# Kernel tuning notes

Hardware: AMD Instinct MI355X
Metric: run time of the kernel (lower is better)

The kernel has to match this reference:

```python
import jax, jax.numpy as jnp
import numpy as np

EMBED = 1024
HEADS = 16
HEAD_DIM = EMBED // HEADS
B, T = 2, 2048


def setup_inputs() -> dict:
    key = jax.random.key(0)
    k1, k2, k3, k4, k5 = jax.random.split(key, 5)
    x = jax.random.normal(k1, (B, T, EMBED), dtype=jnp.float32)
    Wq = jax.random.normal(k2, (HEADS, EMBED, HEAD_DIM), dtype=jnp.float32)
    Wk = jax.random.normal(k3, (HEADS, EMBED, HEAD_DIM), dtype=jnp.float32)
    Wv = jax.random.normal(k4, (HEADS, EMBED, HEAD_DIM), dtype=jnp.float32)
    # nn.Linear weight is [out_features, in_features]
    Wo = jax.random.normal(k5, (EMBED, EMBED), dtype=jnp.float32) * (1.0 / np.sqrt(EMBED))
    return {"x": x, "Wq": Wq, "Wk": Wk, "Wv": Wv, "Wo": Wo}


def reference(x, Wq, Wk, Wv, Wo):
    b, t, e = x.shape
    h, _, i = Wq.shape
    q = jnp.einsum('hei,bte->hbti', Wq, x)
    k = jnp.einsum('hei,bte->hbti', Wk, x)
    v = jnp.einsum('hei,bte->hbti', Wv, x)
    # NOTE: original module scales by sqrt(seq_len), not sqrt(head_dim)
    fit = jnp.einsum('hbti,hbsi->hbts', q, k) / jnp.sqrt(jnp.float32(t))
    fit = jax.nn.softmax(fit, axis=-1)
    attended = jnp.einsum('hbts,hbsi->hbti', fit, v)
    # rearrange 'h b t i -> b t (h i)'
    attended = attended.transpose(1, 2, 0, 3).reshape(b, t, h * i)
    return attended @ Wo.T
```

## Files before the change

### kernel.cpp

```cpp
#include <hip/hip_runtime.h>
#include <math.h>

#define E_DIM 1024
#define H_NUM 16
#define HD 64
#define B_NUM 2
#define T_LEN 2048

typedef unsigned short u16;
typedef short bf16x8 __attribute__((ext_vector_type(8)));
typedef float f32x4 __attribute__((ext_vector_type(4)));
typedef unsigned short u16x4 __attribute__((ext_vector_type(4)));
typedef unsigned short u16x8 __attribute__((ext_vector_type(8)));
typedef unsigned int u32x2 __attribute__((ext_vector_type(2)));

#define MFMA16(a, b, c) __builtin_amdgcn_mfma_f32_16x16x32_bf16(a, b, c, 0, 0, 0)

__device__ __forceinline__ u16 f2bf(float f) {
    unsigned u = __float_as_uint(f);
    u += 0x7FFFu + ((u >> 16) & 1u);
    return (u16)(u >> 16);
}
__device__ __forceinline__ float bf2f(u16 b) {
    return __uint_as_float(((unsigned)b) << 16);
}
__device__ __forceinline__ void gl_lds16(const void* g, void* l) {
    __builtin_amdgcn_global_load_lds(
        (const __attribute__((address_space(1))) unsigned int*)g,
        (__attribute__((address_space(3))) unsigned int*)l, 16, 0, 0);
}


__global__ __launch_bounds__(256) void convert_x_kernel(
    const float* __restrict__ x, u16* __restrict__ xh, u16* __restrict__ xl)
{
    int i = (blockIdx.x * 256 + threadIdx.x) * 4;
    float4 f = *(const float4*)&x[i];
    float fv[4] = {f.x, f.y, f.z, f.w};
    u16x4 h, l;
    #pragma unroll
    for (int j = 0; j < 4; j++) {
        u16 hi = f2bf(fv[j]);
        h[j] = hi;
        l[j] = f2bf(fv[j] - bf2f(hi));
    }
    *(u16x4*)&xh[i] = h;
    *(u16x4*)&xl[i] = l;
}

__global__ __launch_bounds__(256) void convert_w_kernel(
    const float* __restrict__ Wq, const float* __restrict__ Wk, const float* __restrict__ Wv,
    u16* __restrict__ wtp_h, u16* __restrict__ wtp_l)
{
    const int bx = blockIdx.x;
    const int m = bx >> 8, h = (bx >> 4) & 15, e0 = (bx & 15) * 64;
    const float* W = (m == 0 ? Wq : (m == 1 ? Wk : Wv));

    __shared__ u16 Th[64][65];
    __shared__ u16 Tl[64][65];
    const int tid = threadIdx.x;

    #pragma unroll
    for (int j = 0; j < 16; j++) {
        int idx = j * 256 + tid;
        int e = idx >> 6, i = idx & 63;
        float f = W[((size_t)h * E_DIM + e0 + e) * HD + i];
        u16 hi = f2bf(f);
        Th[i][e] = hi;
        Tl[i][e] = f2bf(f - bf2f(hi));
    }
    __syncthreads();
    #pragma unroll
    for (int rep = 0; rep < 2; rep++) {
        int c = rep * 256 + tid;
        int ct_loc = c >> 7, ke_loc = (c >> 6) & 1, lane = c & 63;
        int col = ct_loc * 16 + (lane & 15);
        int el  = ke_loc * 32 + (lane >> 4) * 8;
        int ct_g = m * 64 + h * 4 + ct_loc;
        int ke_g = (bx & 15) * 2 + ke_loc;
        size_t off = ((size_t)ct_g * 32 + ke_g) * 512 + (size_t)lane * 8;
        *(u16x8*)&wtp_h[off] = *(u16x8*)&Th[col][el];
        *(u16x8*)&wtp_l[off] = *(u16x8*)&Tl[col][el];
    }
}

__global__ __launch_bounds__(256) void convert_wo_kernel(
    const float* __restrict__ Wo, u16* __restrict__ wop)
{
    int c = blockIdx.x * 256 + threadIdx.x;
    int lane = c & 63, ke = (c >> 6) & 31, ct = c >> 11;
    int row = ct * 16 + (lane & 15);
    int e   = ke * 32 + (lane >> 4) * 8;
    const float* src = &Wo[(size_t)row * E_DIM + e];
    float4 f0 = *(const float4*)&src[0];
    float4 f1 = *(const float4*)&src[4];
    float fv[8] = {f0.x, f0.y, f0.z, f0.w, f1.x, f1.y, f1.z, f1.w};
    u16x8 hv;
    #pragma unroll
    for (int j = 0; j < 8; j++) hv[j] = f2bf(fv[j]);
    *(u16x8*)&wop[(size_t)c * 8] = hv;
}

__global__ __launch_bounds__(256, 3) void qkv_mfma_kernel(
    const u16* __restrict__ xh, const u16* __restrict__ xl,
    const u16* __restrict__ wtp_h, const u16* __restrict__ wtp_l,
    u16* __restrict__ qp_h, u16* __restrict__ qp_l,
    u16* __restrict__ kp_h, u16* __restrict__ kp_l,
    u16* __restrict__ vp)
{
    const int bx = blockIdx.x;
    const int r0 = blockIdx.y * 128;
    const int m  = bx >> 3;

    __shared__ __align__(16) u16 SM[17408];
    u16* Ah = SM;
    u16* Al = SM + 4096;
    u16* Bh = SM + 8192;
    u16* Bl = SM + 12288;

    const int tid = threadIdx.x;
    const int w = tid >> 6, lane = tid & 63;
    const int qd = lane >> 4, n16 = lane & 15;
    const int wr = w >> 1, wc = w & 1;

    f32x4 acc[4][4];
    #pragma unroll
    for (int i = 0; i < 4; i++)
        #pragma unroll
        for (int j = 0; j < 4; j++) acc[i][j] = (f32x4){0.f, 0.f, 0.f, 0.f};

    for (int k0 = 0; k0 < E_DIM; k0 += 32) {
        __syncthreads();
        const int ke = k0 >> 5;
        #pragma unroll
        for (int rep = 0; rep < 2; rep++) {
            int c = rep * 256 + tid;
            int mt = c >> 6;
            int cl = c & 63;
            int cn = cl & 15, cq = cl >> 4;
            size_t aoff = (size_t)(r0 + mt * 16 + cn) * E_DIM + k0 + cq * 8;
            gl_lds16(&xh[aoff], &Ah[c * 8]);
            gl_lds16(&xl[aoff], &Al[c * 8]);
        }
        #pragma unroll
        for (int rep = 0; rep < 2; rep++) {
            int c = rep * 256 + tid;
            int ct_loc = c >> 6;
            int cl = c & 63;
            size_t boff = ((size_t)(bx * 8 + ct_loc) * 32 + ke) * 512 + (size_t)cl * 8;
            gl_lds16(&wtp_h[boff], &Bh[c * 8]);
            gl_lds16(&wtp_l[boff], &Bl[c * 8]);
        }
        __syncthreads();

        bf16x8 ah[4], al_[4];
        #pragma unroll
        for (int i = 0; i < 4; i++) {
            ah[i]  = *(bf16x8*)&Ah[((wr * 4 + i) * 64 + lane) * 8];
            al_[i] = *(bf16x8*)&Al[((wr * 4 + i) * 64 + lane) * 8];
        }
        #pragma unroll
        for (int j = 0; j < 4; j++) {
            bf16x8 bh = *(bf16x8*)&Bh[((wc * 4 + j) * 64 + lane) * 8];
            bf16x8 bl = *(bf16x8*)&Bl[((wc * 4 + j) * 64 + lane) * 8];
            #pragma unroll
            for (int i = 0; i < 4; i++) {
                acc[i][j] = MFMA16(ah[i], bh, acc[i][j]);
                acc[i][j] = MFMA16(al_[i], bh, acc[i][j]);
                acc[i][j] = MFMA16(ah[i], bl, acc[i][j]);
            }
        }
    }

    const int b  = r0 >> 11;
    const int tloc0 = r0 & 2047;

    if (m == 2) {
        const int h0 = (bx & 7) * 2;
        __syncthreads();
        const int VS = 136;
        u16* TR = SM + wc * 8704;
        #pragma unroll
        for (int i = 0; i < 4; i++) {
            int tl = wr * 64 + i * 16 + qd * 4;
            #pragma unroll
            for (int j = 0; j < 4; j++) {
                int d = j * 16 + n16;
                u16x4 pv;
                #pragma unroll
                for (int r = 0; r < 4; r++) pv[r] = f2bf(acc[i][j][r]);
                *(u16x4*)&TR[d * VS + tl] = pv;
            }
        }
        __syncthreads();
        const int st_g0 = tloc0 >> 6;
        #pragma unroll
        for (int rep = 0; rep < 8; rep++) {
            int c = rep * 256 + tid;
            int hh = c >> 10;
            int idx = c & 1023;
            int st_loc = idx >> 9, ks = (idx >> 8) & 1, dt = (idx >> 6) & 3, cl = idx & 63;
            int d  = dt * 16 + (cl & 15);
            int tl = st_loc * 64 + ks * 32 + (cl >> 4) * 8;
            u16x8 v8 = *(u16x8*)&SM[hh * 8704 + d * VS + tl];
            int hbv = (h0 + hh) * 2 + b;
            size_t off = ((((size_t)hbv * 32 + st_g0 + st_loc) * 2 + ks) * 4 + dt) * 512
                       + (size_t)cl * 8;
            *(u16x8*)&vp[off] = v8;
        }
    } else {
        const int h0 = (bx & 7) * 2;
        const float sc = (m == 0) ? 0.031882937f : 1.0f;
        u16* oh = (m == 0) ? qp_h : kp_h;
        u16* ol = (m == 0) ? qp_l : kp_l;
        const int hb = (h0 + wc) * 2 + b;
        #pragma unroll
        for (int i = 0; i < 4; i++) {
            int nt = (tloc0 >> 4) + wr * 4 + i;
            #pragma unroll
            for (int j = 0; j < 4; j++) {
                int ks = j >> 1;
                int lp = (((j & 1) * 2 + (n16 >> 3)) << 4);
                int pos = n16 & 7;
                size_t cb = (((size_t)hb * 128 + nt) * 2 + ks) * 512;
                #pragma unroll
                for (int r = 0; r < 4; r++) {
                    float f = acc[i][j][r] * sc;
                    u16 hi = f2bf(f);
                    size_t o = cb + (size_t)(lp | (qd * 4 + r)) * 8 + pos;
                    oh[o] = hi;
                    ol[o] = f2bf(f - bf2f(hi));
                }
            }
        }
    }
}

__global__ __launch_bounds__(256) void attn_kernel(
    const u16* __restrict__ qp_h, const u16* __restrict__ qp_l,
    const u16* __restrict__ kp_h, const u16* __restrict__ kp_l,
    const u16* __restrict__ vp, u16* __restrict__ attb)
{
    const int hb = blockIdx.x;
    const int h = hb >> 1, b = hb & 1;
    const int t0 = blockIdx.y * 64;

    __shared__ __align__(16) u16 BKh[4096], BKl[4096];
    __shared__ __align__(16) u16 PT[4][16][72];

    const int tid  = threadIdx.x;
    const int lane = tid & 63;
    const int w    = tid >> 6;
    const int qd   = lane >> 4;
    const int n16  = lane & 15;

    bf16x8 bqh[2], bql[2];
    {
        int qt = (t0 >> 4) + w;
        #pragma unroll
        for (int ks = 0; ks < 2; ks++) {
            size_t off = (((size_t)hb * 128 + qt) * 2 + ks) * 512 + (size_t)lane * 8;
            bqh[ks] = *(const bf16x8*)&qp_h[off];
            bql[ks] = *(const bf16x8*)&qp_l[off];
        }
    }

    f32x4 o4[4];
    #pragma unroll
    for (int dt = 0; dt < 4; dt++) o4[dt] = (f32x4){0.f, 0.f, 0.f, 0.f};
    float mr = -1e30f, lr = 0.f;

    {
        const size_t kb = (size_t)hb * 128 * 2 * 512;
        #pragma unroll
        for (int rep = 0; rep < 2; rep++) {
            int c = rep * 256 + tid;
            gl_lds16(&kp_h[kb + (size_t)c * 8], &BKh[c * 8]);
            gl_lds16(&kp_l[kb + (size_t)c * 8], &BKl[c * 8]);
        }
    }

    for (int st = 0; st < T_LEN / 64; st++) {
        __syncthreads();

        bf16x8 av[4][2];
        #pragma unroll
        for (int ks = 0; ks < 2; ks++)
            #pragma unroll
            for (int dt = 0; dt < 4; dt++) {
                size_t off = ((((size_t)hb * 32 + st) * 2 + ks) * 4 + dt) * 512 + (size_t)lane * 8;
                av[dt][ks] = *(const bf16x8*)&vp[off];
            }

        f32x4 s[4];
        #pragma unroll
        for (int c = 0; c < 4; c++) s[c] = (f32x4){0.f, 0.f, 0.f, 0.f};
        #pragma unroll
        for (int ks = 0; ks < 2; ks++) {
            #pragma unroll
            for (int c = 0; c < 4; c++) {
                bf16x8 akh = *(bf16x8*)&BKh[((c * 2 + ks) * 64 + lane) * 8];
                bf16x8 akl = *(bf16x8*)&BKl[((c * 2 + ks) * 64 + lane) * 8];
                s[c] = MFMA16(akh, bqh[ks], s[c]);
                s[c] = MFMA16(akh, bql[ks], s[c]);
                s[c] = MFMA16(akl, bqh[ks], s[c]);
            }
        }

        __syncthreads();

        if (st + 1 < T_LEN / 64) {
            const size_t kb = ((size_t)hb * 128 + (st + 1) * 4) * 2 * 512;
            #pragma unroll
            for (int rep = 0; rep < 2; rep++) {
                int c = rep * 256 + tid;
                gl_lds16(&kp_h[kb + (size_t)c * 8], &BKh[c * 8]);
                gl_lds16(&kp_l[kb + (size_t)c * 8], &BKl[c * 8]);
            }
        }

        float tmax = s[0][0];
        #pragma unroll
        for (int c = 0; c < 4; c++)
            #pragma unroll
            for (int r = 0; r < 4; r++) tmax = fmaxf(tmax, s[c][r]);
        tmax = fmaxf(tmax, __shfl_xor(tmax, 16));
        tmax = fmaxf(tmax, __shfl_xor(tmax, 32));
        float nm = fmaxf(mr, tmax);
        float al = __builtin_amdgcn_exp2f(mr - nm);
        mr = nm;

        float psum = 0.f;
        #pragma unroll
        for (int c = 0; c < 4; c++) {
            float p0 = __builtin_amdgcn_exp2f(s[c][0] - nm);
            float p1 = __builtin_amdgcn_exp2f(s[c][1] - nm);
            float p2 = __builtin_amdgcn_exp2f(s[c][2] - nm);
            float p3 = __builtin_amdgcn_exp2f(s[c][3] - nm);
            psum += (p0 + p1) + (p2 + p3);
            u32x2 pk;
            pk[0] = (__float_as_uint(p0) >> 16) | (__float_as_uint(p1) & 0xFFFF0000u);
            pk[1] = (__float_as_uint(p2) >> 16) | (__float_as_uint(p3) & 0xFFFF0000u);
            *(u32x2*)&PT[w][n16][c * 16 + qd * 4] = pk;
        }
        if (__any(al != 1.0f)) {
            lr *= al;
            #pragma unroll
            for (int dt = 0; dt < 4; dt++)
                #pragma unroll
                for (int r = 0; r < 4; r++) o4[dt][r] *= al;
        }
        lr += psum;

        #pragma unroll
        for (int ks = 0; ks < 2; ks++) {
            bf16x8 bp = *(bf16x8*)&PT[w][n16][ks * 32 + qd * 8];
            #pragma unroll
            for (int dt = 0; dt < 4; dt++)
                o4[dt] = MFMA16(av[dt][ks], bp, o4[dt]);
        }
    }

    lr += __shfl_xor(lr, 16);
    lr += __shfl_xor(lr, 32);
    float inv = 1.f / lr;
    int row = t0 + w * 16 + n16;
    #pragma unroll
    for (int dt = 0; dt < 4; dt++) {
        u16x4 ov;
        #pragma unroll
        for (int r = 0; r < 4; r++) ov[r] = f2bf(o4[dt][r] * inv);
        *(u16x4*)&attb[(size_t)(b * T_LEN + row) * E_DIM + h * HD + dt * 16 + qd * 4] = ov;
    }
}

__global__ __launch_bounds__(256) void outproj_mfma_kernel(
    const u16* __restrict__ attb, const u16* __restrict__ wop,
    float* __restrict__ out)
{
    const int c0 = blockIdx.x * 64;
    const int r0 = blockIdx.y * 128;

    __shared__ __align__(16) u16 As[8192];

    const int tid = threadIdx.x;
    const int w = tid >> 6, lane = tid & 63;
    const int qd = lane >> 4, n16 = lane & 15;
    const int wr = w >> 1, wc = w & 1;

    f32x4 acc[4][2];
    #pragma unroll
    for (int i = 0; i < 4; i++)
        #pragma unroll
        for (int j = 0; j < 2; j++) acc[i][j] = (f32x4){0.f, 0.f, 0.f, 0.f};

    for (int k0 = 0; k0 < E_DIM; k0 += 64) {
        __syncthreads();
        #pragma unroll
        for (int rep = 0; rep < 4; rep++) {
            int c = rep * 256 + tid;
            int mt = c >> 7, ks = (c >> 6) & 1;
            int cl = c & 63;
            int cn = cl & 15, cq = cl >> 4;
            gl_lds16(&attb[(size_t)(r0 + mt * 16 + cn) * E_DIM + k0 + ks * 32 + cq * 8],
                     &As[c * 8]);
        }
        bf16x8 bb[2][2];
        #pragma unroll
        for (int j = 0; j < 2; j++) {
            int ct = (c0 >> 4) + wc * 2 + j;
            #pragma unroll
            for (int ks = 0; ks < 2; ks++) {
                int ke = (k0 >> 5) + ks;
                bb[j][ks] = *(const bf16x8*)&wop[((size_t)ct * 32 + ke) * 512 + (size_t)lane * 8];
            }
        }
        __syncthreads();

        #pragma unroll
        for (int ks = 0; ks < 2; ks++) {
            bf16x8 a[4];
            #pragma unroll
            for (int i = 0; i < 4; i++)
                a[i] = *(bf16x8*)&As[(((wr * 4 + i) * 2 + ks) * 64 + lane) * 8];
            #pragma unroll
            for (int j = 0; j < 2; j++)
                #pragma unroll
                for (int i = 0; i < 4; i++)
                    acc[i][j] = MFMA16(a[i], bb[j][ks], acc[i][j]);
        }
    }

    #pragma unroll
    for (int i = 0; i < 4; i++) {
        #pragma unroll
        for (int r = 0; r < 4; r++) {
            int row = r0 + wr * 64 + i * 16 + qd * 4 + r;
            #pragma unroll
            for (int j = 0; j < 2; j++) {
                int col = c0 + wc * 32 + j * 16 + n16;
                out[(size_t)row * E_DIM + col] = acc[i][j][r];
            }
        }
    }
}

extern "C" void kernel_launch(void* const* d_in, const int* in_sizes, int n_in,
                              void* d_out, int out_size, void* d_ws, size_t ws_size,
                              hipStream_t stream)
{
    const float* x  = (const float*)d_in[0];
    const float* Wq = (const float*)d_in[1];
    const float* Wk = (const float*)d_in[2];
    const float* Wv = (const float*)d_in[3];
    const float* Wo = (const float*)d_in[4];
    float* out = (float*)d_out;

    const size_t NX = (size_t)4096 * 1024;
    const size_t NW = (size_t)3072 * 1024;
    const size_t NO = (size_t)1024 * 1024;
    const size_t NQ = (size_t)H_NUM * B_NUM * T_LEN * HD;

    u16* xh   = (u16*)d_ws;
    u16* xl   = xh + NX;
    u16* wtph = xl + NX;
    u16* wtpl = wtph + NW;
    u16* wop  = wtpl + NW;
    u16* qph  = wop + NO;
    u16* qpl  = qph + NQ;
    u16* kph  = qpl + NQ;
    u16* kpl  = kph + NQ;
    u16* vp   = kpl + NQ;
    u16* attb = xh;

    convert_x_kernel<<<4096, 256, 0, stream>>>(x, xh, xl);
    convert_w_kernel<<<768, 256, 0, stream>>>(Wq, Wk, Wv, wtph, wtpl);
    convert_wo_kernel<<<512, 256, 0, stream>>>(Wo, wop);

    dim3 g1(24, 32);
    qkv_mfma_kernel<<<g1, 256, 0, stream>>>(xh, xl, wtph, wtpl, qph, qpl, kph, kpl, vp);

    dim3 g2(H_NUM * B_NUM, T_LEN / 64);
    attn_kernel<<<g2, 256, 0, stream>>>(qph, qpl, kph, kpl, vp, attb);

    dim3 g3(E_DIM / 64, 4096 / 128);
    outproj_mfma_kernel<<<g3, 256, 0, stream>>>(attb, wop, out);
}
```

Before: 278.3 us.

## Merge conversion kernels, drop split-bf16 for V, double-buffer K tiles in attention

Merges the three fp32-to-bf16 conversion launches into one kernel that dispatches on block index. In the QKV projection, the V slice now uses a single bf16 MFMA and skips loading the low-order x and weight parts, cutting its MFMA count and traffic to a third. The attention kernel double-buffers the K tile in LDS so the next tile's load overlaps the current QK^T compute, with one barrier per step instead of two. This raises LDS use in attention and lowers V precision, which was already stored as single bf16.

```diff
diff --git a/kernel.cpp b/kernel.cpp
--- a/kernel.cpp
+++ b/kernel.cpp
@@ -31,74 +31,74 @@
 }
 
 
-__global__ __launch_bounds__(256) void convert_x_kernel(
-    const float* __restrict__ x, u16* __restrict__ xh, u16* __restrict__ xl)
+__global__ __launch_bounds__(256) void convert_all_kernel(
+    const float* __restrict__ x,
+    const float* __restrict__ Wq, const float* __restrict__ Wk, const float* __restrict__ Wv,
+    const float* __restrict__ Wo,
+    u16* __restrict__ xh, u16* __restrict__ xl,
+    u16* __restrict__ wtp_h, u16* __restrict__ wtp_l,
+    u16* __restrict__ wop)
 {
-    int i = (blockIdx.x * 256 + threadIdx.x) * 4;
-    float4 f = *(const float4*)&x[i];
-    float fv[4] = {f.x, f.y, f.z, f.w};
-    u16x4 h, l;
-    #pragma unroll
-    for (int j = 0; j < 4; j++) {
-        u16 hi = f2bf(fv[j]);
-        h[j] = hi;
-        l[j] = f2bf(fv[j] - bf2f(hi));
-    }
-    *(u16x4*)&xh[i] = h;
-    *(u16x4*)&xl[i] = l;
-}
-
-__global__ __launch_bounds__(256) void convert_w_kernel(
-    const float* __restrict__ Wq, const float* __restrict__ Wk, const float* __restrict__ Wv,
-    u16* __restrict__ wtp_h, u16* __restrict__ wtp_l)
-{
-    const int bx = blockIdx.x;
-    const int m = bx >> 8, h = (bx >> 4) & 15, e0 = (bx & 15) * 64;
-    const float* W = (m == 0 ? Wq : (m == 1 ? Wk : Wv));
-
-    __shared__ u16 Th[64][65];
-    __shared__ u16 Tl[64][65];
+    const int bid = blockIdx.x;
     const int tid = threadIdx.x;
 
-    #pragma unroll
-    for (int j = 0; j < 16; j++) {
-        int idx = j * 256 + tid;
-        int e = idx >> 6, i = idx & 63;
-        float f = W[((size_t)h * E_DIM + e0 + e) * HD + i];
-        u16 hi = f2bf(f);
-        Th[i][e] = hi;
-        Tl[i][e] = f2bf(f - bf2f(hi));
-    }
-    __syncthreads();
-    #pragma unroll
-    for (int rep = 0; rep < 2; rep++) {
-        int c = rep * 256 + tid;
-        int ct_loc = c >> 7, ke_loc = (c >> 6) & 1, lane = c & 63;
-        int col = ct_loc * 16 + (lane & 15);
-        int el  = ke_loc * 32 + (lane >> 4) * 8;
-        int ct_g = m * 64 + h * 4 + ct_loc;
-        int ke_g = (bx & 15) * 2 + ke_loc;
-        size_t off = ((size_t)ct_g * 32 + ke_g) * 512 + (size_t)lane * 8;
-        *(u16x8*)&wtp_h[off] = *(u16x8*)&Th[col][el];
-        *(u16x8*)&wtp_l[off] = *(u16x8*)&Tl[col][el];
-    }
-}
-
-__global__ __launch_bounds__(256) void convert_wo_kernel(
-    const float* __restrict__ Wo, u16* __restrict__ wop)
-{
-    int c = blockIdx.x * 256 + threadIdx.x;
-    int lane = c & 63, ke = (c >> 6) & 31, ct = c >> 11;
-    int row = ct * 16 + (lane & 15);
-    int e   = ke * 32 + (lane >> 4) * 8;
-    const float* src = &Wo[(size_t)row * E_DIM + e];
-    float4 f0 = *(const float4*)&src[0];
-    float4 f1 = *(const float4*)&src[4];
-    float fv[8] = {f0.x, f0.y, f0.z, f0.w, f1.x, f1.y, f1.z, f1.w};
-    u16x8 hv;
-    #pragma unroll
-    for (int j = 0; j < 8; j++) hv[j] = f2bf(fv[j]);
-    *(u16x8*)&wop[(size_t)c * 8] = hv;
+    if (bid < 4096) {
+        int i = (bid * 256 + tid) * 4;
+        float4 f = *(const float4*)&x[i];
+        float fv[4] = {f.x, f.y, f.z, f.w};
+        u16x4 h, l;
+        #pragma unroll
+        for (int j = 0; j < 4; j++) {
+            u16 hi = f2bf(fv[j]);
+            h[j] = hi;
+            l[j] = f2bf(fv[j] - bf2f(hi));
+        }
+        *(u16x4*)&xh[i] = h;
+        *(u16x4*)&xl[i] = l;
+    } else if (bid < 4096 + 768) {
+        const int bx = bid - 4096;
+        const int m = bx >> 8, h = (bx >> 4) & 15, e0 = (bx & 15) * 64;
+        const float* W = (m == 0 ? Wq : (m == 1 ? Wk : Wv));
+
+        __shared__ u16 Th[64][65];
+        __shared__ u16 Tl[64][65];
+
+        #pragma unroll
+        for (int j = 0; j < 16; j++) {
+            int idx = j * 256 + tid;
+            int e = idx >> 6, i = idx & 63;
+            float f = W[((size_t)h * E_DIM + e0 + e) * HD + i];
+            u16 hi = f2bf(f);
+            Th[i][e] = hi;
+            Tl[i][e] = f2bf(f - bf2f(hi));
+        }
+        __syncthreads();
+        #pragma unroll
+        for (int rep = 0; rep < 2; rep++) {
+            int c = rep * 256 + tid;
+            int ct_loc = c >> 7, ke_loc = (c >> 6) & 1, lane = c & 63;
+            int col = ct_loc * 16 + (lane & 15);
+            int el  = ke_loc * 32 + (lane >> 4) * 8;
+            int ct_g = m * 64 + h * 4 + ct_loc;
+            int ke_g = (bx & 15) * 2 + ke_loc;
+            size_t off = ((size_t)ct_g * 32 + ke_g) * 512 + (size_t)lane * 8;
+            *(u16x8*)&wtp_h[off] = *(u16x8*)&Th[col][el];
+            *(u16x8*)&wtp_l[off] = *(u16x8*)&Tl[col][el];
+        }
+    } else {
+        int c = (bid - 4096 - 768) * 256 + tid;
+        int lane = c & 63, ke = (c >> 6) & 31, ct = c >> 11;
+        int row = ct * 16 + (lane & 15);
+        int e   = ke * 32 + (lane >> 4) * 8;
+        const float* src = &Wo[(size_t)row * E_DIM + e];
+        float4 f0 = *(const float4*)&src[0];
+        float4 f1 = *(const float4*)&src[4];
+        float fv[8] = {f0.x, f0.y, f0.z, f0.w, f1.x, f1.y, f1.z, f1.w};
+        u16x8 hv;
+        #pragma unroll
+        for (int j = 0; j < 8; j++) hv[j] = f2bf(fv[j]);
+        *(u16x8*)&wop[(size_t)c * 8] = hv;
+    }
 }
 
 __global__ __launch_bounds__(256, 3) void qkv_mfma_kernel(
@@ -111,6 +111,7 @@
     const int bx = blockIdx.x;
     const int r0 = blockIdx.y * 128;
     const int m  = bx >> 3;
+    const bool lo = (m != 2);
 
     __shared__ __align__(16) u16 SM[17408];
     u16* Ah = SM;
@@ -140,7 +141,7 @@
             int cn = cl & 15, cq = cl >> 4;
             size_t aoff = (size_t)(r0 + mt * 16 + cn) * E_DIM + k0 + cq * 8;
             gl_lds16(&xh[aoff], &Ah[c * 8]);
-            gl_lds16(&xl[aoff], &Al[c * 8]);
+            if (lo) gl_lds16(&xl[aoff], &Al[c * 8]);
         }
         #pragma unroll
         for (int rep = 0; rep < 2; rep++) {
@@ -149,25 +150,31 @@
             int cl = c & 63;
             size_t boff = ((size_t)(bx * 8 + ct_loc) * 32 + ke) * 512 + (size_t)cl * 8;
             gl_lds16(&wtp_h[boff], &Bh[c * 8]);
-            gl_lds16(&wtp_l[boff], &Bl[c * 8]);
+            if (lo) gl_lds16(&wtp_l[boff], &Bl[c * 8]);
         }
         __syncthreads();
 
         bf16x8 ah[4], al_[4];
         #pragma unroll
         for (int i = 0; i < 4; i++) {
-            ah[i]  = *(bf16x8*)&Ah[((wr * 4 + i) * 64 + lane) * 8];
-            al_[i] = *(bf16x8*)&Al[((wr * 4 + i) * 64 + lane) * 8];
+            ah[i] = *(bf16x8*)&Ah[((wr * 4 + i) * 64 + lane) * 8];
+            if (lo) al_[i] = *(bf16x8*)&Al[((wr * 4 + i) * 64 + lane) * 8];
         }
         #pragma unroll
         for (int j = 0; j < 4; j++) {
             bf16x8 bh = *(bf16x8*)&Bh[((wc * 4 + j) * 64 + lane) * 8];
-            bf16x8 bl = *(bf16x8*)&Bl[((wc * 4 + j) * 64 + lane) * 8];
-            #pragma unroll
-            for (int i = 0; i < 4; i++) {
-                acc[i][j] = MFMA16(ah[i], bh, acc[i][j]);
-                acc[i][j] = MFMA16(al_[i], bh, acc[i][j]);
-                acc[i][j] = MFMA16(ah[i], bl, acc[i][j]);
+            if (lo) {
+                bf16x8 bl = *(bf16x8*)&Bl[((wc * 4 + j) * 64 + lane) * 8];
+                #pragma unroll
+                for (int i = 0; i < 4; i++) {
+                    acc[i][j] = MFMA16(ah[i], bh, acc[i][j]);
+                    acc[i][j] = MFMA16(al_[i], bh, acc[i][j]);
+                    acc[i][j] = MFMA16(ah[i], bl, acc[i][j]);
+                }
+            } else {
+                #pragma unroll
+                for (int i = 0; i < 4; i++)
+                    acc[i][j] = MFMA16(ah[i], bh, acc[i][j]);
             }
         }
     }
@@ -245,7 +252,8 @@
     const int h = hb >> 1, b = hb & 1;
     const int t0 = blockIdx.y * 64;
 
-    __shared__ __align__(16) u16 BKh[4096], BKl[4096];
+    __shared__ __align__(16) u16 BKh0[4096], BKl0[4096];
+    __shared__ __align__(16) u16 BKh1[4096], BKl1[4096];
     __shared__ __align__(16) u16 PT[4][16][72];
 
     const int tid  = threadIdx.x;
@@ -275,20 +283,31 @@
         #pragma unroll
         for (int rep = 0; rep < 2; rep++) {
             int c = rep * 256 + tid;
-            gl_lds16(&kp_h[kb + (size_t)c * 8], &BKh[c * 8]);
-            gl_lds16(&kp_l[kb + (size_t)c * 8], &BKl[c * 8]);
-        }
-    }
-
-    for (int st = 0; st < T_LEN / 64; st++) {
-        __syncthreads();
+            gl_lds16(&kp_h[kb + (size_t)c * 8], &BKh0[c * 8]);
+            gl_lds16(&kp_l[kb + (size_t)c * 8], &BKl0[c * 8]);
+        }
+    }
+
+    auto step = [&](int st, u16* RDh, u16* RDl, u16* WRh, u16* WRl) {
+        __syncthreads();
+
+        if (st + 1 < T_LEN / 64) {
+            const size_t kb = ((size_t)hb * 128 + (st + 1) * 4) * 2 * 512;
+            #pragma unroll
+            for (int rep = 0; rep < 2; rep++) {
+                int c = rep * 256 + tid;
+                gl_lds16(&kp_h[kb + (size_t)c * 8], &WRh[c * 8]);
+                gl_lds16(&kp_l[kb + (size_t)c * 8], &WRl[c * 8]);
+            }
+        }
 
         bf16x8 av[4][2];
         #pragma unroll
         for (int ks = 0; ks < 2; ks++)
             #pragma unroll
             for (int dt = 0; dt < 4; dt++) {
-                size_t off = ((((size_t)hb * 32 + st) * 2 + ks) * 4 + dt) * 512 + (size_t)lane * 8;
+                size_t off = ((((size_t)hb * 32 + st) * 2 + ks) * 4 + dt) * 512
+                           + (size_t)lane * 8;
                 av[dt][ks] = *(const bf16x8*)&vp[off];
             }
 
@@ -299,23 +318,11 @@
         for (int ks = 0; ks < 2; ks++) {
             #pragma unroll
             for (int c = 0; c < 4; c++) {
-                bf16x8 akh = *(bf16x8*)&BKh[((c * 2 + ks) * 64 + lane) * 8];
-                bf16x8 akl = *(bf16x8*)&BKl[((c * 2 + ks) * 64 + lane) * 8];
+                bf16x8 akh = *(bf16x8*)&RDh[((c * 2 + ks) * 64 + lane) * 8];
+                bf16x8 akl = *(bf16x8*)&RDl[((c * 2 + ks) * 64 + lane) * 8];
                 s[c] = MFMA16(akh, bqh[ks], s[c]);
                 s[c] = MFMA16(akh, bql[ks], s[c]);
                 s[c] = MFMA16(akl, bqh[ks], s[c]);
-            }
-        }
-
-        __syncthreads();
-
-        if (st + 1 < T_LEN / 64) {
-            const size_t kb = ((size_t)hb * 128 + (st + 1) * 4) * 2 * 512;
-            #pragma unroll
-            for (int rep = 0; rep < 2; rep++) {
-                int c = rep * 256 + tid;
-                gl_lds16(&kp_h[kb + (size_t)c * 8], &BKh[c * 8]);
-                gl_lds16(&kp_l[kb + (size_t)c * 8], &BKl[c * 8]);
             }
         }
 
@@ -359,6 +366,11 @@
             for (int dt = 0; dt < 4; dt++)
                 o4[dt] = MFMA16(av[dt][ks], bp, o4[dt]);
         }
+    };
+
+    for (int i = 0; i < T_LEN / 128; i++) {
+        step(2 * i,     BKh0, BKl0, BKh1, BKl1);
+        step(2 * i + 1, BKh1, BKl1, BKh0, BKl0);
     }
 
     lr += __shfl_xor(lr, 16);
@@ -473,9 +485,8 @@
     u16* vp   = kpl + NQ;
     u16* attb = xh;
 
-    convert_x_kernel<<<4096, 256, 0, stream>>>(x, xh, xl);
-    convert_w_kernel<<<768, 256, 0, stream>>>(Wq, Wk, Wv, wtph, wtpl);
-    convert_wo_kernel<<<512, 256, 0, stream>>>(Wo, wop);
+    convert_all_kernel<<<4096 + 768 + 512, 256, 0, stream>>>(
+        x, Wq, Wk, Wv, Wo, xh, xl, wtph, wtpl, wop);
 
     dim3 g1(24, 32);
     qkv_mfma_kernel<<<g1, 256, 0, stream>>>(xh, xl, wtph, wtpl, qph, qpl, kph, kpl, vp);
```

Result: faster. 259.4 us (-6.8%).
